# Optimization experiments

Measured on AMD Instinct MI355X. Metric: run time of the kernel, lower is better.

Reference implementation:

```python
import jax, jax.numpy as jnp
import numpy as np

B, SQ, SK = 2, 2048, 2048
DQ = DK = DV = DM = DOUT = 1024
H = 16
DHEAD = DM // H


def setup_inputs() -> dict:
    key = jax.random.key(0)
    ks = jax.random.split(key, 12)
    s = 0.02
    return {
        "Q": jax.random.normal(ks[0], (B, SQ, DQ), jnp.float32),
        "K": jax.random.normal(ks[1], (B, SK, DK), jnp.float32),
        "V": jax.random.normal(ks[2], (B, SK, DV), jnp.float32),
        "mask": jax.random.randint(ks[3], (B, 1, SK), 0, 2, jnp.int32),
        "Wq": jax.random.normal(ks[4], (DQ, DM), jnp.float32) * s,
        "bq": jnp.zeros((DM,), jnp.float32),
        "Wk": jax.random.normal(ks[5], (DK, DM), jnp.float32) * s,
        "bk": jnp.zeros((DM,), jnp.float32),
        "Wv": jax.random.normal(ks[6], (DV, DM), jnp.float32) * s,
        "bv": jnp.zeros((DM,), jnp.float32),
        "Wo": jax.random.normal(ks[7], (DM, DOUT), jnp.float32) * s,
        "bo": jnp.zeros((DOUT,), jnp.float32),
    }


def reference(Q, K, V, mask, Wq, bq, Wk, bk, Wv, bv, Wo, bo):
    b, sq, _ = Q.shape
    # QKV projections then split heads: (B, S, D) -> (B, H, S, d_k)
    q = (Q @ Wq + bq).reshape(b, sq, H, DHEAD).transpose(0, 2, 1, 3)
    k = (K @ Wk + bk).reshape(b, -1, H, DHEAD).transpose(0, 2, 1, 3)
    v = (V @ Wv + bv).reshape(b, -1, H, DHEAD).transpose(0, 2, 1, 3)
    # scores: (B, H, Sq, Sk)
    scores = jnp.einsum("bhqd,bhkd->bhqk", q, k) / np.sqrt(DHEAD).astype(np.float32)
    m = mask[:, None]  # (B,1,1,Sk), broadcast over heads and queries
    scores = jnp.where(m == 0, -jnp.inf, scores)
    attn = jax.nn.softmax(scores, axis=-1)
    out = jnp.einsum("bhqk,bhkd->bhqd", attn, v)
    out = out.transpose(0, 2, 1, 3).reshape(b, sq, DM)
    return out @ Wo + bo
```

## Files before the change

### kernel.cpp

```cpp
#include <hip/hip_runtime.h>
#include <hip/hip_bf16.h>

#define SQn 2048
#define SKn 2048
#define DMn 1024
#define NHn 16
#define DHn 64

typedef __attribute__((ext_vector_type(8))) short bf16x8;
typedef __attribute__((ext_vector_type(4))) float f32x4;

#define QSCALE 0.1803368801f

__device__ __forceinline__ short f2bf(float f) {
  union { float f; unsigned u; } a; a.f = f;
  return (short)((a.u + 0x7FFFu + ((a.u >> 16) & 1u)) >> 16);
}

__device__ __forceinline__ unsigned cvt_pk_bf16(float lo, float hi) {
  unsigned r;
  asm("v_cvt_pk_bf16_f32 %0, %1, %2" : "=v"(r) : "v"(lo), "v"(hi));
  return r;
}

__device__ __forceinline__ void gload16(const void* g, void* l) {
  __builtin_amdgcn_global_load_lds(
      (__attribute__((address_space(1))) void*)g,
      (__attribute__((address_space(3))) void*)l, 16, 0, 0);
}

#define NCASTB 12288
__global__ __launch_bounds__(256) void prep(
    const float* __restrict__ Q, const float* __restrict__ K, const float* __restrict__ V,
    const float* __restrict__ W0, const float* __restrict__ W1,
    const float* __restrict__ W2, const float* __restrict__ W3,
    const int* __restrict__ mask,
    short* __restrict__ qkvOut, short* __restrict__ WtBase,
    int* __restrict__ pos, int* __restrict__ Lb) {
  const int blk = blockIdx.x;
  const int tid = threadIdx.x;
  __shared__ float t[32][33];
  __shared__ int part[256];
  __shared__ int base[256];

  if (blk < NCASTB) {
    const int n4each = (2 * 2048 * 1024) / 4;
    int i = blk * 256 + tid;
    const float* src;
    int j = i;
    if (i < n4each) src = Q;
    else if (i < 2 * n4each) { src = K; j = i - n4each; }
    else { src = V; j = i - 2 * n4each; }
    float4 f = ((const float4*)src)[j];
    short4 o;
    o.x = f2bf(f.x); o.y = f2bf(f.y); o.z = f2bf(f.z); o.w = f2bf(f.w);
    ((short4*)qkvOut)[i] = o;
  } else if (blk < NCASTB + 4096) {
    const int tt = blk - NCASTB;
    const int z = tt >> 10;
    const int rem = tt & 1023;
    const float* W = (z == 0) ? W0 : (z == 1) ? W1 : (z == 2) ? W2 : W3;
    short* Wt = WtBase + (size_t)z * DMn * DMn;
    const int bx = (rem & 31) * 32;
    const int by = (rem >> 5) * 32;
    const int tx = tid & 31, ty = tid >> 5;
#pragma unroll
    for (int j = 0; j < 4; ++j)
      t[ty + j * 8][tx] = W[(size_t)(by + ty + j * 8) * DMn + bx + tx];
    __syncthreads();
#pragma unroll
    for (int j = 0; j < 4; ++j)
      Wt[(size_t)(bx + ty + j * 8) * DMn + by + tx] = f2bf(t[tx][ty + j * 8]);
  } else {
    const int b = blk - NCASTB - 4096;
    const int* m = mask + b * SKn;
    int v[8];
    int s0 = 0;
#pragma unroll
    for (int j = 0; j < 8; ++j) { v[j] = m[tid * 8 + j] ? 1 : 0; s0 += v[j]; }
    part[tid] = s0;
    __syncthreads();
    if (tid == 0) {
      int acc = 0;
      for (int i = 0; i < 256; ++i) { base[i] = acc; acc += part[i]; }
      Lb[b] = acc;
    }
    __syncthreads();
    int acc = base[tid];
    int* p = pos + b * SKn;
#pragma unroll
    for (int j = 0; j < 8; ++j) { p[tid * 8 + j] = acc; acc += v[j]; }
  }
}

__global__ __launch_bounds__(512) void gemm_bt3(
    const short* __restrict__ A0, const short* __restrict__ A1, const short* __restrict__ A2,
    const short* __restrict__ B0, const short* __restrict__ B1, const short* __restrict__ B2,
    const float* __restrict__ c0, const float* __restrict__ c1, const float* __restrict__ c2,
    short* __restrict__ O0, short* __restrict__ O1, short* __restrict__ O2,
    const int* __restrict__ maskp, const int* __restrict__ posp,
    const int* __restrict__ Lp) {
  constexpr int K = 1024;
  const int z = blockIdx.z;
  const short* A  = (z == 0) ? A0 : (z == 1) ? A1 : A2;
  const short* Bt = (z == 0) ? B0 : (z == 1) ? B1 : B2;
  const float* bias = (z == 0) ? c0 : (z == 1) ? c1 : c2;
  short* Cout = (z == 0) ? O0 : (z == 1) ? O1 : O2;

  __shared__ short As[128 * 32];
  __shared__ short Bs[128 * 32];
  const int tid = threadIdx.x;
  const int lane = tid & 63;
  const int wid = tid >> 6;
  const int wr = wid >> 2, wc = wid & 3;
  const int bm = blockIdx.x * 128, bn = blockIdx.y * 128;

  f32x4 acc[4][2] = {};

  const int srow = tid >> 2;
  const int scol = (tid & 3) * 8;
  const short* Ag = A + (size_t)bm * K;
  const short* Bg = Bt + (size_t)bn * K;

  for (int k0 = 0; k0 < K; k0 += 32) {
    __syncthreads();
    gload16(Ag + (size_t)srow * K + k0 + scol, As + tid * 8);
    gload16(Bg + (size_t)srow * K + k0 + scol, Bs + tid * 8);
    __syncthreads();

    bf16x8 a[4], b[2];
    const int rowA = wr * 64 + (lane & 15);
    const int rowB = wc * 32 + (lane & 15);
    const int ko = (lane >> 4) * 8;
#pragma unroll
    for (int m = 0; m < 4; ++m) a[m] = *(const bf16x8*)(As + (rowA + m * 16) * 32 + ko);
#pragma unroll
    for (int n = 0; n < 2; ++n) b[n] = *(const bf16x8*)(Bs + (rowB + n * 16) * 32 + ko);
#pragma unroll
    for (int m = 0; m < 4; ++m)
#pragma unroll
      for (int n = 0; n < 2; ++n)
        acc[m][n] = __builtin_amdgcn_mfma_f32_16x16x32_bf16(a[m], b[n], acc[m][n], 0, 0, 0);
  }

  const int crow0 = bm + wr * 64 + ((lane >> 4) * 4);
  const int ccol0 = bn + wc * 32 + (lane & 15);
  float bv[2];
#pragma unroll
  for (int n = 0; n < 2; ++n) bv[n] = bias[ccol0 + n * 16];
#pragma unroll
  for (int m = 0; m < 4; ++m)
#pragma unroll
    for (int i = 0; i < 4; ++i) {
      int row = crow0 + m * 16 + i;
      int bb = row >> 11, s = row & 2047;
      if (z != 0) {
        int mm = maskp[(bb << 11) + s];
        int pp = posp[(bb << 11) + s];
        s = mm ? pp : (Lp[bb] + s - pp);
      }
#pragma unroll
      for (int n = 0; n < 2; ++n) {
        int col = ccol0 + n * 16;
        float val = acc[m][n][i] + bv[n];
        int hh = col >> 6, d = col & 63;
        if (z == 2) {
          Cout[((((size_t)bb * NHn + hh) * DHn + d) << 11) + s] = f2bf(val);
        } else {
          if (z == 0) val *= QSCALE;
          Cout[((((size_t)bb * NHn + hh) * SQn + s) << 6) + d] = f2bf(val);
        }
      }
    }
}

__global__ __launch_bounds__(512) void gemm_n64(const short* __restrict__ A,
                                                const short* __restrict__ Bt,
                                                const float* __restrict__ bias,
                                                float* __restrict__ C) {
  constexpr int K = 1024, N = 1024;
  __shared__ short As[128 * 32];
  __shared__ short Bs[64 * 32];
  const int tid = threadIdx.x;
  const int lane = tid & 63;
  const int wid = tid >> 6;
  const int wr = wid >> 1, wc = wid & 1;
  const int bm = blockIdx.x * 128, bn = blockIdx.y * 64;

  f32x4 acc[2][2] = {};

  const int srow = tid >> 2;
  const int scol = (tid & 3) * 8;
  const short* Ag = A + (size_t)bm * K;
  const short* Bg = Bt + (size_t)bn * K;

  for (int k0 = 0; k0 < K; k0 += 32) {
    __syncthreads();
    gload16(Ag + (size_t)srow * K + k0 + scol, As + tid * 8);
    if (tid < 256)
      gload16(Bg + (size_t)srow * K + k0 + scol, Bs + tid * 8);
    __syncthreads();

    bf16x8 a[2], b[2];
    const int rowA = wr * 32 + (lane & 15);
    const int rowB = wc * 32 + (lane & 15);
    const int ko = (lane >> 4) * 8;
#pragma unroll
    for (int m = 0; m < 2; ++m) a[m] = *(const bf16x8*)(As + (rowA + m * 16) * 32 + ko);
#pragma unroll
    for (int n = 0; n < 2; ++n) b[n] = *(const bf16x8*)(Bs + (rowB + n * 16) * 32 + ko);
#pragma unroll
    for (int m = 0; m < 2; ++m)
#pragma unroll
      for (int n = 0; n < 2; ++n)
        acc[m][n] = __builtin_amdgcn_mfma_f32_16x16x32_bf16(a[m], b[n], acc[m][n], 0, 0, 0);
  }

  const int crow0 = bm + wr * 32 + ((lane >> 4) * 4);
  const int ccol0 = bn + wc * 32 + (lane & 15);
#pragma unroll
  for (int m = 0; m < 2; ++m)
#pragma unroll
    for (int n = 0; n < 2; ++n) {
      int col = ccol0 + n * 16;
      float bv = bias[col];
#pragma unroll
      for (int i = 0; i < 4; ++i) {
        int row = crow0 + m * 16 + i;
        C[(size_t)row * N + col] = acc[m][n][i] + bv;
      }
    }
}

__global__ __launch_bounds__(512) void attn(const short* __restrict__ q,
                                            const short* __restrict__ k,
                                            const short* __restrict__ vt,
                                            const int* __restrict__ Lb,
                                            short* __restrict__ out) {
  __shared__ short Ks[2][64 * 64];
  __shared__ short Vs[2][64 * 64];
  __shared__ short Ps[8][16 * 64];

  const int tid = threadIdx.x;
  const int lane = tid & 63;
  const int w = tid >> 6;
  const int l = (blockIdx.x & 7) * 64 + (blockIdx.x >> 3);
  const int bh = l >> 4;
  const int qt = l & 15;
  const int h = bh & 15;
  const int b = bh >> 4;
  const size_t hoff = (size_t)bh * (SQn * DHn);

  const int c_ = lane & 15, g_ = lane >> 4;
  const int swz = (c_ & 7) << 4;

  const int L = Lb[b];
  const int nt = (L + 63) >> 6;
  const int lastt = nt - 1;

  bf16x8 qf[2];
  {
    const short* qp = q + hoff + (size_t)(qt * 128 + w * 16 + c_) * DHn + g_ * 8;
    qf[0] = *(const bf16x8*)qp;
    qf[1] = *(const bf16x8*)(qp + 32);
  }

  const int r0 = tid >> 3;
  const int gch = (tid & 7) ^ (r0 & 7);
  const size_t kO = (size_t)r0 * DHn + gch * 8;
  const size_t vO = (size_t)r0 * SKn + gch * 8;
  const int ldsO = tid * 8;

  float mrun = -1e30f;
  float lrun = 0.f;
  f32x4 o[4] = {};
  char* PwB = (char*)Ps[w];

#define STAGE(buf, kbase, vbase)            \
  gload16((kbase) + kO, &Ks[buf][ldsO]);    \
  gload16((vbase) + vO, &Vs[buf][ldsO]);

  const short* kpre = k + hoff;
  const short* vpre = vt + hoff;
  STAGE(0, kpre, vpre);
  kpre += 64 * DHn;
  vpre += 64;
  __syncthreads();

  int cur = 0;
  for (int kt = 0; kt < nt; ++kt) {
    if (kt + 1 < nt) {
      STAGE(cur ^ 1, kpre, vpre);
      kpre += 64 * DHn;
      vpre += 64;
    }

    const short* Kc = Ks[cur];
    const short* Vc = Vs[cur];

    f32x4 s[4];
    __builtin_amdgcn_s_setprio(1);
#pragma unroll
    for (int n = 0; n < 4; ++n) {
      f32x4 a = {};
      int key = n * 16 + c_;
#pragma unroll
      for (int kc = 0; kc < 2; ++kc) {
        int slot = (kc * 4 + g_) ^ (key & 7);
        bf16x8 kf = *(const bf16x8*)(Kc + key * 64 + slot * 8);
        a = __builtin_amdgcn_mfma_f32_16x16x32_bf16(kf, qf[kc], a, 0, 0, 0);
      }
      s[n] = a;
    }
    __builtin_amdgcn_s_setprio(0);

    if (kt == lastt) {
      const int kb = kt * 64 + g_ * 4;
#pragma unroll
      for (int n = 0; n < 4; ++n) {
        const int k0i = kb + n * 16;
        s[n][0] = (k0i + 0 < L) ? s[n][0] : -1e30f;
        s[n][1] = (k0i + 1 < L) ? s[n][1] : -1e30f;
        s[n][2] = (k0i + 2 < L) ? s[n][2] : -1e30f;
        s[n][3] = (k0i + 3 < L) ? s[n][3] : -1e30f;
      }
    }

    float pmax = fmaxf(fmaxf(s[0][0], s[0][1]), fmaxf(s[0][2], s[0][3]));
#pragma unroll
    for (int n = 1; n < 4; ++n)
      pmax = fmaxf(pmax, fmaxf(fmaxf(s[n][0], s[n][1]), fmaxf(s[n][2], s[n][3])));

    if (!__all(pmax - mrun <= 8.f)) {
      float pm = fmaxf(pmax, __shfl_xor(pmax, 16));
      pm = fmaxf(pm, __shfl_xor(pm, 32));
      float mn = fmaxf(mrun, pm);
      float sc = __builtin_amdgcn_exp2f(mrun - mn);
      mrun = mn;
      lrun *= sc;
      float scB[4];
#pragma unroll
      for (int i = 0; i < 4; ++i) scB[i] = __shfl(sc, g_ * 4 + i);
#pragma unroll
      for (int n = 0; n < 4; ++n)
#pragma unroll
        for (int i = 0; i < 4; ++i) o[n][i] *= scB[i];
    }

    float lsum = 0.f;
#pragma unroll
    for (int n = 0; n < 4; ++n) {
      float p0 = __builtin_amdgcn_exp2f(s[n][0] - mrun);
      float p1 = __builtin_amdgcn_exp2f(s[n][1] - mrun);
      float p2 = __builtin_amdgcn_exp2f(s[n][2] - mrun);
      float p3 = __builtin_amdgcn_exp2f(s[n][3] - mrun);
      lsum += (p0 + p1) + (p2 + p3);
      uint2 pk;
      pk.x = cvt_pk_bf16(p0, p1);
      pk.y = cvt_pk_bf16(p2, p3);
      *(uint2*)(PwB + ((c_ * 128) | ((n * 32 + g_ * 8) ^ swz))) = pk;
    }
    lrun += lsum;

    __builtin_amdgcn_s_setprio(1);
#pragma unroll
    for (int ks = 0; ks < 2; ++ks) {
      bf16x8 pf = *(const bf16x8*)(PwB + ((c_ * 128) | ((ks * 64 + g_ * 16) ^ swz)));
#pragma unroll
      for (int n = 0; n < 4; ++n) {
        int d = n * 16 + c_;
        int slot = (ks * 4 + g_) ^ (d & 7);
        bf16x8 vf = *(const bf16x8*)(Vc + d * 64 + slot * 8);
        o[n] = __builtin_amdgcn_mfma_f32_16x16x32_bf16(pf, vf, o[n], 0, 0, 0);
      }
    }
    __builtin_amdgcn_s_setprio(0);

    __syncthreads();
    cur ^= 1;
  }

  lrun += __shfl_xor(lrun, 16);
  lrun += __shfl_xor(lrun, 32);
  float lB[4];
#pragma unroll
  for (int i = 0; i < 4; ++i) lB[i] = __shfl(lrun, g_ * 4 + i);
#pragma unroll
  for (int n = 0; n < 4; ++n) {
#pragma unroll
    for (int i = 0; i < 4; ++i) {
      int srow = qt * 128 + w * 16 + g_ * 4 + i;
      int d = n * 16 + c_;
      out[((size_t)b * SQn + srow) * DMn + h * 64 + d] = f2bf(o[n][i] / lB[i]);
    }
  }
#undef STAGE
}

extern "C" void kernel_launch(void* const* d_in, const int* in_sizes, int n_in,
                              void* d_out, int out_size, void* d_ws, size_t ws_size,
                              hipStream_t stream) {
  const float* Q  = (const float*)d_in[0];
  const float* K  = (const float*)d_in[1];
  const float* V  = (const float*)d_in[2];
  const int* mask = (const int*)d_in[3];
  const float* Wq = (const float*)d_in[4];
  const float* bq = (const float*)d_in[5];
  const float* Wk = (const float*)d_in[6];
  const float* bk = (const float*)d_in[7];
  const float* Wv = (const float*)d_in[8];
  const float* bv = (const float*)d_in[9];
  const float* Wo = (const float*)d_in[10];
  const float* bo = (const float*)d_in[11];

  char* ws = (char*)d_ws;
  const size_t MB = 1024 * 1024;
  short* Qb  = (short*)(ws + 0 * MB);
  short* Wqt = (short*)(ws + 24 * MB);
  short* Wkt = (short*)(ws + 26 * MB);
  short* Wvt = (short*)(ws + 28 * MB);
  short* Wot = (short*)(ws + 30 * MB);
  short* qp  = (short*)(ws + 32 * MB);
  short* kp  = (short*)(ws + 40 * MB);
  short* vpt = (short*)(ws + 48 * MB);
  int*   posp = (int*)(ws + 56 * MB);
  int*   Lbp  = (int*)(ws + 56 * MB + 16384);
  short* Kb  = Qb + 4 * MB;
  short* Vb  = Qb + 8 * MB;
  short* ao  = Qb;

  prep<<<NCASTB + 4096 + 2, 256, 0, stream>>>(Q, K, V, Wq, Wk, Wv, Wo, mask,
                                              Qb, Wqt, posp, Lbp);

  gemm_bt3<<<dim3(32, 8, 3), 512, 0, stream>>>(Qb, Kb, Vb, Wqt, Wkt, Wvt,
                                               bq, bk, bv, qp, kp, vpt,
                                               mask, posp, Lbp);

  attn<<<512, 512, 0, stream>>>(qp, kp, vpt, Lbp, ao);

  gemm_n64<<<dim3(32, 16), 512, 0, stream>>>(ao, Wot, bo, (float*)d_out);
}
```

Measured before the change: 118.6 us.

## Double-buffer LDS staging in projection GEMMs and shrink output GEMM block

Both the fused QKV projection GEMM and the output projection GEMM now double-buffer their LDS tiles. Global-to-LDS loads for the next two k-steps are issued ahead, with explicit vmcnt waits and raw s_barrier in place of two __syncthreads per iteration, and MFMA issue gets raised priority. The output GEMM also drops to 256 threads per block, with each wave computing a 64x32 tile (4x2 MFMAs) instead of 32x32. The aim is to hide global load latency behind MFMA work and cut barrier overhead. In exchange, LDS use doubles, and the hand-tuned vmcnt counts depend on exactly how the loads are issued.

Result: no change. 117.2 us (-1.2%).

```diff
diff --git a/kernel.cpp b/kernel.cpp
--- a/kernel.cpp
+++ b/kernel.cpp
@@ -11,6 +11,11 @@
 typedef __attribute__((ext_vector_type(4))) float f32x4;
 
 #define QSCALE 0.1803368801f
+
+#define FBAR()                                     \
+  __builtin_amdgcn_sched_barrier(0);               \
+  asm volatile("s_barrier" ::: "memory");          \
+  __builtin_amdgcn_sched_barrier(0)
 
 __device__ __forceinline__ short f2bf(float f) {
   union { float f; unsigned u; } a; a.f = f;
@@ -107,8 +112,8 @@
   const float* bias = (z == 0) ? c0 : (z == 1) ? c1 : c2;
   short* Cout = (z == 0) ? O0 : (z == 1) ? O1 : O2;
 
-  __shared__ short As[128 * 32];
-  __shared__ short Bs[128 * 32];
+  __shared__ short As[2][128 * 32];
+  __shared__ short Bs[2][128 * 32];
   const int tid = threadIdx.x;
   const int lane = tid & 63;
   const int wid = tid >> 6;
@@ -122,26 +127,40 @@
   const short* Ag = A + (size_t)bm * K;
   const short* Bg = Bt + (size_t)bn * K;
 
-  for (int k0 = 0; k0 < K; k0 += 32) {
-    __syncthreads();
-    gload16(Ag + (size_t)srow * K + k0 + scol, As + tid * 8);
-    gload16(Bg + (size_t)srow * K + k0 + scol, Bs + tid * 8);
-    __syncthreads();
+#define GSTG(buf, k0)                                              \
+  gload16(Ag + (size_t)srow * K + (k0) + scol, As[buf] + tid * 8); \
+  gload16(Bg + (size_t)srow * K + (k0) + scol, Bs[buf] + tid * 8);
+
+  GSTG(0, 0);
+  GSTG(1, 32);
+
+  const int rowA = wr * 64 + (lane & 15);
+  const int rowB = wc * 32 + (lane & 15);
+  const int ko = (lane >> 4) * 8;
+
+  for (int t = 0; t < 32; ++t) {
+    const int cur = t & 1;
+    if (t < 31) asm volatile("s_waitcnt vmcnt(2)" ::: "memory");
+    else        asm volatile("s_waitcnt vmcnt(0)" ::: "memory");
+    FBAR();
 
     bf16x8 a[4], b[2];
-    const int rowA = wr * 64 + (lane & 15);
-    const int rowB = wc * 32 + (lane & 15);
-    const int ko = (lane >> 4) * 8;
-#pragma unroll
-    for (int m = 0; m < 4; ++m) a[m] = *(const bf16x8*)(As + (rowA + m * 16) * 32 + ko);
-#pragma unroll
-    for (int n = 0; n < 2; ++n) b[n] = *(const bf16x8*)(Bs + (rowB + n * 16) * 32 + ko);
+#pragma unroll
+    for (int m = 0; m < 4; ++m) a[m] = *(const bf16x8*)(As[cur] + (rowA + m * 16) * 32 + ko);
+#pragma unroll
+    for (int n = 0; n < 2; ++n) b[n] = *(const bf16x8*)(Bs[cur] + (rowB + n * 16) * 32 + ko);
+    __builtin_amdgcn_s_setprio(1);
 #pragma unroll
     for (int m = 0; m < 4; ++m)
 #pragma unroll
       for (int n = 0; n < 2; ++n)
         acc[m][n] = __builtin_amdgcn_mfma_f32_16x16x32_bf16(a[m], b[n], acc[m][n], 0, 0, 0);
-  }
+    __builtin_amdgcn_s_setprio(0);
+
+    FBAR();
+    if (t < 30) { GSTG(cur, t * 32 + 64); }
+  }
+#undef GSTG
 
   const int crow0 = bm + wr * 64 + ((lane >> 4) * 4);
   const int ccol0 = bn + wc * 32 + (lane & 15);
@@ -174,52 +193,66 @@
     }
 }
 
-__global__ __launch_bounds__(512) void gemm_n64(const short* __restrict__ A,
+__global__ __launch_bounds__(256) void gemm_n64(const short* __restrict__ A,
                                                 const short* __restrict__ Bt,
                                                 const float* __restrict__ bias,
                                                 float* __restrict__ C) {
   constexpr int K = 1024, N = 1024;
-  __shared__ short As[128 * 32];
-  __shared__ short Bs[64 * 32];
+  __shared__ short As[2][128 * 32];
+  __shared__ short Bs[2][64 * 32];
   const int tid = threadIdx.x;
   const int lane = tid & 63;
   const int wid = tid >> 6;
   const int wr = wid >> 1, wc = wid & 1;
   const int bm = blockIdx.x * 128, bn = blockIdx.y * 64;
 
-  f32x4 acc[2][2] = {};
+  f32x4 acc[4][2] = {};
 
   const int srow = tid >> 2;
   const int scol = (tid & 3) * 8;
   const short* Ag = A + (size_t)bm * K;
   const short* Bg = Bt + (size_t)bn * K;
 
-  for (int k0 = 0; k0 < K; k0 += 32) {
-    __syncthreads();
-    gload16(Ag + (size_t)srow * K + k0 + scol, As + tid * 8);
-    if (tid < 256)
-      gload16(Bg + (size_t)srow * K + k0 + scol, Bs + tid * 8);
-    __syncthreads();
-
-    bf16x8 a[2], b[2];
-    const int rowA = wr * 32 + (lane & 15);
-    const int rowB = wc * 32 + (lane & 15);
-    const int ko = (lane >> 4) * 8;
-#pragma unroll
-    for (int m = 0; m < 2; ++m) a[m] = *(const bf16x8*)(As + (rowA + m * 16) * 32 + ko);
-#pragma unroll
-    for (int n = 0; n < 2; ++n) b[n] = *(const bf16x8*)(Bs + (rowB + n * 16) * 32 + ko);
-#pragma unroll
-    for (int m = 0; m < 2; ++m)
+#define GSTG(buf, k0)                                                             \
+  gload16(Ag + (size_t)srow * K + (k0) + scol,        As[buf] + tid * 8);         \
+  gload16(Ag + (size_t)(srow + 64) * K + (k0) + scol, As[buf] + 2048 + tid * 8);  \
+  gload16(Bg + (size_t)srow * K + (k0) + scol,        Bs[buf] + tid * 8);
+
+  GSTG(0, 0);
+  GSTG(1, 32);
+
+  const int rowA = wr * 64 + (lane & 15);
+  const int rowB = wc * 32 + (lane & 15);
+  const int ko = (lane >> 4) * 8;
+
+  for (int t = 0; t < 32; ++t) {
+    const int cur = t & 1;
+    if (t < 31) asm volatile("s_waitcnt vmcnt(3)" ::: "memory");
+    else        asm volatile("s_waitcnt vmcnt(0)" ::: "memory");
+    FBAR();
+
+    bf16x8 a[4], b[2];
+#pragma unroll
+    for (int m = 0; m < 4; ++m) a[m] = *(const bf16x8*)(As[cur] + (rowA + m * 16) * 32 + ko);
+#pragma unroll
+    for (int n = 0; n < 2; ++n) b[n] = *(const bf16x8*)(Bs[cur] + (rowB + n * 16) * 32 + ko);
+    __builtin_amdgcn_s_setprio(1);
+#pragma unroll
+    for (int m = 0; m < 4; ++m)
 #pragma unroll
       for (int n = 0; n < 2; ++n)
         acc[m][n] = __builtin_amdgcn_mfma_f32_16x16x32_bf16(a[m], b[n], acc[m][n], 0, 0, 0);
-  }
-
-  const int crow0 = bm + wr * 32 + ((lane >> 4) * 4);
+    __builtin_amdgcn_s_setprio(0);
+
+    FBAR();
+    if (t < 30) { GSTG(cur, t * 32 + 64); }
+  }
+#undef GSTG
+
+  const int crow0 = bm + wr * 64 + ((lane >> 4) * 4);
   const int ccol0 = bn + wc * 32 + (lane & 15);
 #pragma unroll
-  for (int m = 0; m < 2; ++m)
+  for (int m = 0; m < 4; ++m)
 #pragma unroll
     for (int n = 0; n < 2; ++n) {
       int col = ccol0 + n * 16;
@@ -438,5 +471,5 @@
 
   attn<<<512, 512, 0, stream>>>(qp, kp, vpt, Lbp, ao);
 
-  gemm_n64<<<dim3(32, 16), 512, 0, stream>>>(ao, Wot, bo, (float*)d_out);
-}
+  gemm_n64<<<dim3(32, 16), 256, 0, stream>>>(ao, Wot, bo, (float*)d_out);
+}
```
